# Kernel tuning notes

Hardware: AMD Instinct MI355X
Metric: run time of the kernel (lower is better)

The kernel has to match this reference:

```python
import jax, jax.numpy as jnp
import numpy as np

C_A = 768; C_S = 384; C_Z = 128; H = 16; D = C_A // H
B = 1; N = 4096; NQ = 32; NK = 128; NB = N // NQ
EPS = 1e-5


def _ln(x):
    # layernorm without learned affine (affine applied by caller where present)
    m = jnp.mean(x, axis=-1, keepdims=True)
    v = jnp.mean((x - m) ** 2, axis=-1, keepdims=True)
    return (x - m) * jax.lax.rsqrt(v + EPS)


def setup_inputs() -> dict:
    key = jax.random.key(0)
    ks = jax.random.split(key, 16)
    w = lambda k, shp: jax.random.normal(k, shp, dtype=jnp.float32) * 0.02
    return dict(
        a=jax.random.normal(ks[0], (B, N, C_A), jnp.float32),
        s=jax.random.normal(ks[1], (B, N, C_S), jnp.float32),
        z=jax.random.normal(ks[2], (B, NB, NQ, NK, C_Z), jnp.float32),
        adaln_gamma_s=jnp.ones((C_S,), jnp.float32),
        adaln_ws=w(ks[3], (C_S, C_A)),
        adaln_bs=jnp.zeros((C_A,), jnp.float32),
        adaln_wskip=w(ks[4], (C_S, C_A)),
        lnz_gamma=jnp.ones((C_Z,), jnp.float32),
        wz=w(ks[5], (C_Z, H)),
        wq=w(ks[6], (C_A, C_A)), bq=jnp.zeros((C_A,), jnp.float32),
        wk=w(ks[7], (C_A, C_A)),
        wv=w(ks[8], (C_A, C_A)),
        wg=w(ks[9], (C_A, C_A)), bg=jnp.ones((C_A,), jnp.float32),
        wo=w(ks[10], (C_A, C_A)), bo=jnp.zeros((C_A,), jnp.float32),
        w_last=w(ks[11], (C_S, C_A)),
        b_last=jnp.full((C_A,), -2.0, jnp.float32),  # biasinit = -2.0
        n_queries=NQ, n_keys=NK,
    )


def _forward(a, s, z, adaln_gamma_s, adaln_ws, adaln_bs, adaln_wskip,
             lnz_gamma, wz, wq, bq, wk, wv, wg, bg, wo, bo,
             w_last, b_last, n_queries, n_keys):
    Bq, Nq, _ = a.shape
    nb = Nq // n_queries
    # AdaptiveLayerNorm (AF3 Alg 26): a <- sigmoid(Lin(s_ln)) * LN(a) + LinNoBias(s_ln)
    s_ln = _ln(s) * adaln_gamma_s
    a_ln = jax.nn.sigmoid(s_ln @ adaln_ws + adaln_bs) * _ln(a) + s_ln @ adaln_wskip
    # pair bias: LN(z) (no offset) -> per-head bias, permuted to [B,H,nb,nq,nk]
    bias = (_ln(z) * lnz_gamma) @ wz                    # [B, nb, nq, nk, H]
    bias = jnp.transpose(bias, (0, 4, 1, 2, 3))          # [B, H, nb, nq, nk]
    # projections (q has bias; k/v no bias)
    q = (a_ln @ wq + bq).reshape(Bq, nb, n_queries, H, D)
    k = (a_ln @ wk).reshape(Bq, Nq, H, D)
    v = (a_ln @ wv).reshape(Bq, Nq, H, D)
    # local window: query block w covers [w*nq, (w+1)*nq); keys are nk centered on it
    start = jnp.arange(nb) * n_queries + n_queries // 2 - n_keys // 2
    kidx = start[:, None] + jnp.arange(n_keys)[None, :]  # [nb, nk]
    valid = (kidx >= 0) & (kidx < Nq)
    kidx = jnp.clip(kidx, 0, Nq - 1)
    k_loc = k[:, kidx]                                    # [B, nb, nk, H, D]
    v_loc = v[:, kidx]
    scale = 1.0 / float(np.sqrt(D))
    scores = jnp.einsum('bwqhd,bwkhd->bhwqk', q, k_loc) * scale + bias
    scores = jnp.where(valid[None, None, :, None, :], scores, -1e9)
    p = jax.nn.softmax(scores, axis=-1)
    o = jnp.einsum('bhwqk,bwkhd->bwqhd', p, v_loc).reshape(Bq, Nq, C_A)
    # gating, output projection, final sigmoid gate from raw s
    o = (jax.nn.sigmoid(a_ln @ wg + bg) * o) @ wo + bo
    return jax.nn.sigmoid(s @ w_last + b_last) * o


def reference(a, s, z, adaln_gamma_s, adaln_ws, adaln_bs, adaln_wskip,
              lnz_gamma, wz, wq, bq, wk, wv, wg, bg, wo, bo,
              w_last, b_last, n_queries, n_keys):
    return _forward(a, s, z, adaln_gamma_s, adaln_ws, adaln_bs, adaln_wskip,
                    lnz_gamma, wz, wq, bq, wk, wv, wg, bg, wo, bo,
                    w_last, b_last, n_queries, n_keys)
```

## Files before the change

### kernel.cpp

```cpp
#include <hip/hip_runtime.h>
#include <hip/hip_bf16.h>
#include <math.h>

#define N_TOK 4096
#define CA 768
#define CS 384
#define CZ 128
#define NHEAD 16
#define DH 48
#define NQW 32
#define NKW 128
#define NBLK 128

typedef __attribute__((ext_vector_type(8))) short short8;
typedef __attribute__((ext_vector_type(4))) float float4v;
typedef __attribute__((ext_vector_type(4))) unsigned short ushort4v;

__device__ __forceinline__ float sigmoidf_(float x){ return 1.0f/(1.0f+__expf(-x)); }

__device__ __forceinline__ unsigned short f2bf(float x){
  unsigned u = __float_as_uint(x);
  unsigned r = (u + 0x7FFFu + ((u>>16)&1u)) >> 16;
  return (unsigned short)r;
}
__device__ __forceinline__ float bf2f(unsigned short b){
  return __uint_as_float(((unsigned)b)<<16);
}
__device__ __forceinline__ short8 cvt8(const float* xv){
  union { short8 v; unsigned short u[8]; } H;
  #pragma unroll
  for (int j=0;j<8;j++) H.u[j] = f2bf(xv[j]);
  return H.v;
}
__device__ __forceinline__ short8 cvt8pk(const float* x){
  union { short8 v; unsigned u32[4]; } H;
  #pragma unroll
  for (int i=0;i<4;i++)
    asm("v_cvt_pk_bf16_f32 %0, %1, %2" : "=v"(H.u32[i]) : "v"(x[2*i]), "v"(x[2*i+1]));
  return H.v;
}

__device__ __forceinline__ void gload_lds16(const void* gsrc, void* ldst){
  __builtin_amdgcn_global_load_lds(
    (const __attribute__((address_space(1))) void*)gsrc,
    (__attribute__((address_space(3))) void*)ldst, 16, 0, 0);
}

__device__ __forceinline__ int xcd_swz(int wg, int nwg){
  int cpx = nwg >> 3;
  return (wg & 7)*cpx + (wg >> 3);
}

__global__ __launch_bounds__(256) void prep_zbias_kernel(
  const float* __restrict__ z, const float* __restrict__ lnz_gamma,
  const float* __restrict__ wz, unsigned short* __restrict__ bias3,
  const float* __restrict__ s, const float* __restrict__ adaln_gamma,
  unsigned short* __restrict__ s_ln_h, unsigned short* __restrict__ s_h,
  const float* __restrict__ a, float* __restrict__ a_n,
  const float* __restrict__ ws, const float* __restrict__ wskip,
  const float* __restrict__ wq, const float* __restrict__ wk,
  const float* __restrict__ wv, const float* __restrict__ wg,
  const float* __restrict__ wo, const float* __restrict__ wlast,
  unsigned short* __restrict__ Wt1, unsigned short* __restrict__ Wt2,
  unsigned short* __restrict__ Wt3, unsigned short* __restrict__ Wt4,
  const float* __restrict__ bq, const float* __restrict__ bg,
  float* __restrict__ biasq)
{
  union PZ {
    float tile[64][65];
    float zbuf[2][2][2048];
  };
  __shared__ PZ sm;
  int bid = blockIdx.x;
  int tid = threadIdx.x;

  if (bid < 2048){
    int wave = tid>>6, lane = tid&63;
    if (wave >= 2) return;
    int lr = lane&15, quad = lane>>4;

    short8 bwh[4];
    float w1 = 0.f;
    #pragma unroll
    for (int ks=0;ks<4;ks++){
      float wv_[8];
      #pragma unroll
      for (int j=0;j<8;j++){
        int k = ks*32 + quad*8 + j;
        wv_[j] = wz[k*NHEAD + lr]*lnz_gamma[k];
        w1 += wv_[j];
      }
      bwh[ks] = cvt8pk(wv_);
    }
    w1 += __shfl_xor(w1, 16);
    w1 += __shfl_xor(w1, 32);

    size_t group = (size_t)bid*2 + wave;
    const float* zg = z + group*(size_t)(NKW*CZ);
    unsigned short* outg = bias3 + group*2048;

    int rsub = lane>>5;
    int csw  = lane&31;
    auto stage = [&](int buf, int b){
      #pragma unroll
      for (int i=0;i<8;i++){
        int r  = 2*i + rsub;
        int gc = csw ^ (r & 7);
        gload_lds16(zg + (size_t)(b*16 + r)*CZ + gc*4, &sm.zbuf[wave][buf][i*256]);
      }
    };

    stage(0, 0);
    int buf = 0;
    #pragma unroll 1
    for (int b=0; b<8; ++b){
      if (b < 7){
        stage(buf^1, b+1);
        asm volatile("s_waitcnt vmcnt(8)" ::: "memory");
      } else {
        asm volatile("s_waitcnt vmcnt(0)" ::: "memory");
      }
      __builtin_amdgcn_sched_barrier(0);

      const float* rowp = &sm.zbuf[wave][buf][lr*128];
      int sswz = lr & 7;
      float4 p[8];
      #pragma unroll
      for (int ks=0;ks<4;ks++){
        int c0 = ks*8 + quad*2;
        p[ks*2]   = *(const float4*)(rowp + (size_t)((c0  )^sswz)*4);
        p[ks*2+1] = *(const float4*)(rowp + (size_t)((c0+1)^sswz)*4);
      }
      float sum=0.f, sq=0.f;
      #pragma unroll
      for (int t=0;t<8;t++){
        sum += p[t].x + p[t].y + p[t].z + p[t].w;
        sq  += p[t].x*p[t].x + p[t].y*p[t].y + p[t].z*p[t].z + p[t].w*p[t].w;
      }
      sum += __shfl_xor(sum,16); sum += __shfl_xor(sum,32);
      sq  += __shfl_xor(sq,16);  sq  += __shfl_xor(sq,32);
      float mean = sum*(1.f/CZ);
      float var  = sq*(1.f/CZ) - mean*mean;
      float rs = rsqrtf(var + 1e-5f);

      float4v c = (float4v){0.f,0.f,0.f,0.f};
      #pragma unroll
      for (int ks=0;ks<4;ks++){
        float xv[8];
        xv[0]=p[ks*2].x;   xv[1]=p[ks*2].y;   xv[2]=p[ks*2].z;   xv[3]=p[ks*2].w;
        xv[4]=p[ks*2+1].x; xv[5]=p[ks*2+1].y; xv[6]=p[ks*2+1].z; xv[7]=p[ks*2+1].w;
        c = __builtin_amdgcn_mfma_f32_16x16x32_bf16(cvt8pk(xv), bwh[ks], c, 0,0,0);
      }

      ushort4v o4;
      #pragma unroll
      for (int r=0;r<4;r++){
        int rrow = quad*4 + r;
        float m_r  = __shfl(mean, rrow);
        float rs_r = __shfl(rs, rrow);
        o4[r] = f2bf(rs_r*(c[r] - m_r*w1));
      }
      *(ushort4v*)(outg + lr*128 + b*16 + quad*4) = o4;
      buf ^= 1;
    }
    return;
  }
  bid -= 2048;

  if (bid < 1024){
    int wave = tid>>6, lane = tid&63;
    int row = bid*4 + wave;
    const float* x = s + (size_t)row*CS;
    float v[6]; float sum=0.f, sq=0.f;
    #pragma unroll
    for (int i=0;i<6;i++){ v[i]=x[lane+64*i]; sum+=v[i]; sq+=v[i]*v[i]; }
    #pragma unroll
    for (int off=32; off; off>>=1){ sum+=__shfl_xor(sum,off); sq+=__shfl_xor(sq,off); }
    float m = sum*(1.f/CS);
    float var = sq*(1.f/CS)-m*m;
    float rs = rsqrtf(var+1e-5f);
    #pragma unroll
    for (int i=0;i<6;i++){
      int c = lane+64*i;
      s_ln_h[(size_t)row*CS+c] = f2bf((v[i]-m)*rs*adaln_gamma[c]);
      s_h[(size_t)row*CS+c]    = f2bf(v[i]);
    }
    return;
  }
  bid -= 1024;

  if (bid < 1024){
    int wave = tid>>6, lane = tid&63;
    int row = bid*4 + wave;
    const float* x = a + (size_t)row*CA;
    float v[12]; float sum=0.f, sq=0.f;
    #pragma unroll
    for (int i=0;i<12;i++){ v[i]=x[lane+64*i]; sum+=v[i]; sq+=v[i]*v[i]; }
    #pragma unroll
    for (int off=32; off; off>>=1){ sum+=__shfl_xor(sum,off); sq+=__shfl_xor(sq,off); }
    float m = sum*(1.f/CA);
    float var = sq*(1.f/CA)-m*m;
    float rs = rsqrtf(var+1e-5f);
    float* o = a_n + (size_t)row*CA;
    #pragma unroll
    for (int i=0;i<12;i++) o[lane+64*i] = (v[i]-m)*rs;
    return;
  }
  bid -= 1024;

  if (bid < 936){
    const float* src; unsigned short* dst; int K; int local;
    if      (bid < 72)  { src=ws;    dst=Wt1;                   K=CS; local=bid; }
    else if (bid < 144) { src=wskip; dst=Wt1 + (size_t)768*CS;  K=CS; local=bid-72; }
    else if (bid < 288) { src=wq;    dst=Wt2;                   K=CA; local=bid-144; }
    else if (bid < 432) { src=wk;    dst=Wt2 + (size_t)768*CA;  K=CA; local=bid-288; }
    else if (bid < 576) { src=wv;    dst=Wt2 + (size_t)1536*CA; K=CA; local=bid-432; }
    else if (bid < 720) { src=wg;    dst=Wt2 + (size_t)2304*CA; K=CA; local=bid-576; }
    else if (bid < 864) { src=wo;    dst=Wt3;                   K=CA; local=bid-720; }
    else                { src=wlast; dst=Wt4;                   K=CS; local=bid-864; }
    int ktiles = K/64;
    int kb = (local % ktiles)*64, nb = (local / ktiles)*64;
    int c = tid & 63, r0 = tid >> 6;
    #pragma unroll
    for (int i=0;i<16;i++){
      int r = r0 + 4*i;
      sm.tile[r][c] = src[(size_t)(kb+r)*CA + nb + c];
    }
    __syncthreads();
    #pragma unroll
    for (int i=0;i<16;i++){
      int r = r0 + 4*i;
      dst[(size_t)(nb+r)*K + kb + c] = f2bf(sm.tile[c][r]);
    }
    return;
  }
  bid -= 936;

  int i = bid*256 + tid;
  float v = 0.f;
  if (i < 768) v = bq[i];
  else if (i >= 2304) v = bg[i-2304];
  biasq[i] = v;
}

__global__ __launch_bounds__(256) void adaln_gemm(
  const unsigned short* __restrict__ A, const unsigned short* __restrict__ Bt,
  const float* __restrict__ bs, const float* __restrict__ a_n,
  unsigned short* __restrict__ outh)
{
  __shared__ unsigned short Ash[64*64];
  __shared__ unsigned short B1sh[128*64];
  __shared__ unsigned short B2sh[128*64];

  int tid = threadIdx.x;
  int w = tid >> 6, lane = tid & 63;
  int lr = lane & 15, quad = lane >> 4;
  int wg = xcd_swz(blockIdx.y*gridDim.x + blockIdx.x, gridDim.x*gridDim.y);
  int bx = wg % gridDim.x, by = wg / gridDim.x;
  int m0 = by*64, n0 = bx*128;
  int mbase = (w&1)*32, nbase = (w>>1)*64;

  float4v acc1[2][4], acc2[2][4];
  #pragma unroll
  for (int i=0;i<2;i++)
    #pragma unroll
    for (int j=0;j<4;j++){
      acc1[i][j] = (float4v){0.f,0.f,0.f,0.f};
      acc2[i][j] = (float4v){0.f,0.f,0.f,0.f};
    }

  int rsub = lane>>3;
  int gcs  = ((lane&7) ^ rsub)*8;
  int rkey = lr & 7;

  for (int k0=0; k0<CS; k0+=64){
    __syncthreads();
    #pragma unroll
    for (int it=0; it<2; ++it){
      int r = it*32 + w*8 + rsub;
      gload_lds16(A + (size_t)(m0 + r)*CS + k0 + gcs, &Ash[(it*32 + w*8)*64]);
    }
    #pragma unroll
    for (int it=0; it<4; ++it){
      int r = it*32 + w*8 + rsub;
      gload_lds16(Bt + (size_t)(n0 + r)*CS + k0 + gcs, &B1sh[(it*32 + w*8)*64]);
      gload_lds16(Bt + (size_t)(768 + n0 + r)*CS + k0 + gcs, &B2sh[(it*32 + w*8)*64]);
    }
    __syncthreads();

    #pragma unroll
    for (int ks=0; ks<2; ++ks){
      int slot = ((ks*4 + quad) ^ rkey)*8;
      short8 af[2], b1f[4], b2f[4];
      #pragma unroll
      for (int mi=0;mi<2;mi++)
        af[mi] = *(const short8*)&Ash[(mbase + mi*16 + lr)*64 + slot];
      #pragma unroll
      for (int ni=0;ni<4;ni++){
        b1f[ni] = *(const short8*)&B1sh[(nbase + ni*16 + lr)*64 + slot];
        b2f[ni] = *(const short8*)&B2sh[(nbase + ni*16 + lr)*64 + slot];
      }
      #pragma unroll
      for (int mi=0;mi<2;mi++)
        #pragma unroll
        for (int ni=0;ni<4;ni++){
          acc1[mi][ni] = __builtin_amdgcn_mfma_f32_16x16x32_bf16(af[mi], b1f[ni], acc1[mi][ni], 0,0,0);
          acc2[mi][ni] = __builtin_amdgcn_mfma_f32_16x16x32_bf16(af[mi], b2f[ni], acc2[mi][ni], 0,0,0);
        }
    }
  }

  #pragma unroll
  for (int ni=0;ni<4;ni++){
    int col = n0 + nbase + ni*16 + lr;
    float bsv = bs[col];
    #pragma unroll
    for (int mi=0;mi<2;mi++){
      #pragma unroll
      for (int reg=0;reg<4;reg++){
        int row = m0 + mbase + mi*16 + quad*4 + reg;
        float v = sigmoidf_(acc1[mi][ni][reg] + bsv)*a_n[(size_t)row*CA + col] + acc2[mi][ni][reg];
        outh[(size_t)row*CA + col] = f2bf(v);
      }
    }
  }
}

__global__ __launch_bounds__(256) void final_gemm(
  const unsigned short* __restrict__ A1, const unsigned short* __restrict__ B1,
  const float* __restrict__ bias1,
  const unsigned short* __restrict__ A2, const unsigned short* __restrict__ B2,
  const float* __restrict__ bias2,
  float* __restrict__ outp)
{
  __shared__ unsigned short Ash[64*64];
  __shared__ unsigned short Bsh[128*64];

  int tid = threadIdx.x;
  int w = tid >> 6, lane = tid & 63;
  int lr = lane & 15, quad = lane >> 4;
  int wg = xcd_swz(blockIdx.y*gridDim.x + blockIdx.x, gridDim.x*gridDim.y);
  int bx = wg % gridDim.x, by = wg / gridDim.x;
  int m0 = by*64, n0 = bx*128;
  int mbase = (w&1)*32, nbase = (w>>1)*64;

  float4v acc1[2][4], acc2[2][4];
  #pragma unroll
  for (int i=0;i<2;i++)
    #pragma unroll
    for (int j=0;j<4;j++){
      acc1[i][j] = (float4v){0.f,0.f,0.f,0.f};
      acc2[i][j] = (float4v){0.f,0.f,0.f,0.f};
    }

  int rsub = lane>>3;
  int gcs  = ((lane&7) ^ rsub)*8;
  int rkey = lr & 7;

  const int NT1 = CA/64, NT2 = CS/64, NT = NT1+NT2;
  #pragma unroll 1
  for (int t=0; t<NT; ++t){
    const unsigned short* Ap; const unsigned short* Bp; int K, k0;
    if (t < NT1){ Ap=A1; Bp=B1; K=CA; k0=t*64; }
    else        { Ap=A2; Bp=B2; K=CS; k0=(t-NT1)*64; }
    __syncthreads();
    #pragma unroll
    for (int it=0; it<2; ++it){
      int r = it*32 + w*8 + rsub;
      gload_lds16(Ap + (size_t)(m0 + r)*K + k0 + gcs, &Ash[(it*32 + w*8)*64]);
    }
    #pragma unroll
    for (int it=0; it<4; ++it){
      int r = it*32 + w*8 + rsub;
      gload_lds16(Bp + (size_t)(n0 + r)*K + k0 + gcs, &Bsh[(it*32 + w*8)*64]);
    }
    __syncthreads();

    #pragma unroll
    for (int ks=0; ks<2; ++ks){
      int slot = ((ks*4 + quad) ^ rkey)*8;
      short8 af[2], bf[4];
      #pragma unroll
      for (int mi=0;mi<2;mi++)
        af[mi] = *(const short8*)&Ash[(mbase + mi*16 + lr)*64 + slot];
      #pragma unroll
      for (int ni=0;ni<4;ni++)
        bf[ni] = *(const short8*)&Bsh[(nbase + ni*16 + lr)*64 + slot];
      if (t < NT1){
        #pragma unroll
        for (int mi=0;mi<2;mi++)
          #pragma unroll
          for (int ni=0;ni<4;ni++)
            acc1[mi][ni] = __builtin_amdgcn_mfma_f32_16x16x32_bf16(af[mi], bf[ni], acc1[mi][ni], 0,0,0);
      } else {
        #pragma unroll
        for (int mi=0;mi<2;mi++)
          #pragma unroll
          for (int ni=0;ni<4;ni++)
            acc2[mi][ni] = __builtin_amdgcn_mfma_f32_16x16x32_bf16(af[mi], bf[ni], acc2[mi][ni], 0,0,0);
      }
    }
  }

  #pragma unroll
  for (int ni=0;ni<4;ni++){
    int col = n0 + nbase + ni*16 + lr;
    float bv1 = bias1[col];
    float bv2 = bias2[col];
    #pragma unroll
    for (int mi=0;mi<2;mi++){
      #pragma unroll
      for (int reg=0;reg<4;reg++){
        int row = m0 + mbase + mi*16 + quad*4 + reg;
        outp[(size_t)row*CA + col] = sigmoidf_(acc2[mi][ni][reg] + bv2)*(acc1[mi][ni][reg] + bv1);
      }
    }
  }
}

__global__ __launch_bounds__(512) void qkvg_gemm256(
  const unsigned short* __restrict__ A1, const unsigned short* __restrict__ B1,
  const float* __restrict__ bias1, unsigned short* __restrict__ outp)
{
  __shared__ unsigned short Ash[2][256*64];
  __shared__ unsigned short Bsh[2][256*64];

  int tid = threadIdx.x;
  int v = tid >> 6, lane = tid & 63;
  int lr = lane & 15, quad = lane >> 4;
  int wg = xcd_swz(blockIdx.y*gridDim.x + blockIdx.x, gridDim.x*gridDim.y);
  int bx = wg % gridDim.x, by = wg / gridDim.x;
  int m0 = by*256, n0 = bx*256;
  int wr = (v>>2)*128;
  int wc = (v&3)*64;

  float4v acc[8][4];
  #pragma unroll
  for (int i=0;i<8;i++)
    #pragma unroll
    for (int j=0;j<4;j++)
      acc[i][j] = (float4v){0.f,0.f,0.f,0.f};

  int rsub = lane>>3;
  int gcs  = ((lane&7) ^ rsub)*8;
  int rkey = lr & 7;

  const int NT = CA/64;

  auto stage = [&](int buf, int t){
    int k0 = t*64;
    #pragma unroll
    for (int i=0;i<4;i++){
      int R = i*64 + v*8;
      gload_lds16(A1 + (size_t)(m0 + R + rsub)*CA + k0 + gcs, &Ash[buf][R*64]);
      gload_lds16(B1 + (size_t)(n0 + R + rsub)*CA + k0 + gcs, &Bsh[buf][R*64]);
    }
  };

  stage(0, 0);
  stage(1, 1);
  int cur = 0;
  #pragma unroll 1
  for (int t=0; t<NT; ++t){
    if (t+1 < NT) asm volatile("s_waitcnt vmcnt(8)" ::: "memory");
    else          asm volatile("s_waitcnt vmcnt(0)" ::: "memory");
    __builtin_amdgcn_sched_barrier(0);
    __builtin_amdgcn_s_barrier();
    #pragma unroll
    for (int ks=0; ks<2; ++ks){
      int slot = ((ks*4 + quad) ^ rkey)*8;
      short8 af[8], bf[4];
      #pragma unroll
      for (int mi=0;mi<8;mi++)
        af[mi] = *(const short8*)&Ash[cur][(wr + mi*16 + lr)*64 + slot];
      #pragma unroll
      for (int ni=0;ni<4;ni++)
        bf[ni] = *(const short8*)&Bsh[cur][(wc + ni*16 + lr)*64 + slot];
      #pragma unroll
      for (int mi=0;mi<8;mi++)
        #pragma unroll
        for (int ni=0;ni<4;ni++)
          acc[mi][ni] = __builtin_amdgcn_mfma_f32_16x16x32_bf16(af[mi], bf[ni], acc[mi][ni], 0,0,0);
    }
    __builtin_amdgcn_s_barrier();
    if (t+2 < NT) stage(cur, t+2);
    cur ^= 1;
  }

  #pragma unroll
  for (int ni=0;ni<4;ni++){
    int col = n0 + wc + ni*16 + lr;
    float bv = bias1[col];
    #pragma unroll
    for (int mi=0;mi<8;mi++){
      #pragma unroll
      for (int reg=0;reg<4;reg++){
        int row = m0 + wr + mi*16 + quad*4 + reg;
        outp[(size_t)row*3072 + col] = f2bf(acc[mi][ni][reg] + bv);
      }
    }
  }
}

__global__ __launch_bounds__(256) void attn_kernel(
  const unsigned short* __restrict__ qh,
  const unsigned short* __restrict__ bias3h,
  unsigned short* __restrict__ og)
{
  __shared__ unsigned short Vs[128*192];
  __shared__ unsigned short Pb[4][32*40];
  int tid = threadIdx.x, wave = tid>>6, lane = tid&63;
  int lr = lane&15, quad = lane>>4;
  int w = blockIdx.x, h = blockIdx.y*4 + wave;
  int start = w*NQW - 48;
  const float scale = 0.14433756729740643f;

  {
    int hbase = blockIdx.y*4*DH;
    #pragma unroll
    for (int it=0; it<12; ++it){
      int c = it*256 + tid;
      int key = c/24, cc = c - key*24;
      int kr = min(max(start+key,0),N_TOK-1);
      short8 v = *(const short8*)&qh[(size_t)kr*3072 + 1536 + hbase + cc*8];
      int cs = cc ^ (((key>>3)&3)*2);
      *(short8*)&Vs[key*192 + cs*8] = v;
    }
  }

  short8 zero8 = {0,0,0,0,0,0,0,0};

  short8 aq[2][2];
  #pragma unroll
  for (int mt=0;mt<2;mt++){
    int row = w*NQW + mt*16 + lr;
    const unsigned short* qp = qh + (size_t)row*3072 + h*DH;
    aq[mt][0] = *(const short8*)(qp + quad*8);
    aq[mt][1] = (quad<2) ? *(const short8*)(qp + 32 + quad*8) : zero8;
  }

  float4v c[2][8];
  #pragma unroll
  for (int mt=0;mt<2;mt++)
    #pragma unroll
    for (int nt=0;nt<8;nt++) c[mt][nt] = (float4v){0.f,0.f,0.f,0.f};

  #pragma unroll 2
  for (int nt=0;nt<8;nt++){
    int krc = min(max(start + nt*16 + lr,0),N_TOK-1);
    const unsigned short* kp = qh + (size_t)krc*3072 + 768 + h*DH;
    short8 bk0 = *(const short8*)(kp + quad*8);
    short8 bk1 = (quad<2) ? *(const short8*)(kp + 32 + quad*8) : zero8;
    #pragma unroll
    for (int mt=0;mt<2;mt++){
      c[mt][nt] = __builtin_amdgcn_mfma_f32_16x16x32_bf16(aq[mt][0], bk0, c[mt][nt], 0,0,0);
      c[mt][nt] = __builtin_amdgcn_mfma_f32_16x16x32_bf16(aq[mt][1], bk1, c[mt][nt], 0,0,0);
    }
  }

  float rmax[2][4], rsum[2][4];
  #pragma unroll
  for (int mt=0;mt<2;mt++)
    #pragma unroll
    for (int r=0;r<4;r++){ rmax[mt][r] = -3.0e38f; rsum[mt][r] = 0.f; }

  #pragma unroll
  for (int nt=0;nt<8;nt++){
    int key = start + nt*16 + lr;
    bool valid = (key>=0) && (key<N_TOK);
    #pragma unroll
    for (int mt=0;mt<2;mt++){
      #pragma unroll
      for (int r=0;r<4;r++){
        int q = mt*16 + quad*4 + r;
        float bv = bf2f(bias3h[(((size_t)(w*NQW+q))*NHEAD + h)*128 + nt*16 + lr]);
        float v = valid ? (c[mt][nt][r]*scale + bv) : -1e9f;
        c[mt][nt][r] = v;
        rmax[mt][r] = fmaxf(rmax[mt][r], v);
      }
    }
  }
  #pragma unroll
  for (int mt=0;mt<2;mt++)
    #pragma unroll
    for (int r=0;r<4;r++){
      float m = rmax[mt][r];
      m = fmaxf(m, __shfl_xor(m,1)); m = fmaxf(m, __shfl_xor(m,2));
      m = fmaxf(m, __shfl_xor(m,4)); m = fmaxf(m, __shfl_xor(m,8));
      rmax[mt][r] = m;
    }
  #pragma unroll
  for (int nt=0;nt<8;nt++)
    #pragma unroll
    for (int mt=0;mt<2;mt++)
      #pragma unroll
      for (int r=0;r<4;r++){
        float e = __expf(c[mt][nt][r] - rmax[mt][r]);
        c[mt][nt][r] = e;
        rsum[mt][r] += e;
      }
  #pragma unroll
  for (int mt=0;mt<2;mt++)
    #pragma unroll
    for (int r=0;r<4;r++){
      float sv = rsum[mt][r];
      sv += __shfl_xor(sv,1); sv += __shfl_xor(sv,2);
      sv += __shfl_xor(sv,4); sv += __shfl_xor(sv,8);
      rsum[mt][r] = 1.f/sv;
    }

  __syncthreads();

  unsigned short* ph = &Pb[wave][0];
  float4v o[2][3];
  #pragma unroll
  for (int mt=0;mt<2;mt++)
    #pragma unroll
    for (int no=0;no<3;no++) o[mt][no] = (float4v){0.f,0.f,0.f,0.f};

  #pragma unroll 1
  for (int c2=0;c2<2;c2++){
    #pragma unroll 1
    for (int ks=0;ks<2;ks++){
      int ntb = c2*4 + ks*2;
      #pragma unroll
      for (int t=0;t<2;t++){
        int nt = ntb + t;
        #pragma unroll
        for (int mt=0;mt<2;mt++){
          #pragma unroll
          for (int r=0;r<4;r++){
            int q = mt*16 + quad*4 + r;
            ph[q*40 + t*16 + lr] = f2bf(c[mt][nt][r]*rsum[mt][r]);
          }
        }
      }
      short8 pa[2];
      #pragma unroll
      for (int mt=0;mt<2;mt++)
        pa[mt] = *(const short8*)&ph[(mt*16+lr)*40 + quad*8];
      #pragma unroll
      for (int no=0;no<3;no++){
        union { short8 v; unsigned short u[8]; } V;
        int col = wave*DH + no*16 + lr;
        int chunk = col >> 3;
        int cs = (chunk ^ (quad*2))*8 + (col & 7);
        #pragma unroll
        for (int j=0;j<8;j++){
          int key = c2*64 + ks*32 + quad*8 + j;
          V.u[j] = Vs[key*192 + cs];
        }
        #pragma unroll
        for (int mt=0;mt<2;mt++)
          o[mt][no] = __builtin_amdgcn_mfma_f32_16x16x32_bf16(pa[mt], V.v, o[mt][no], 0,0,0);
      }
    }
  }

  #pragma unroll
  for (int mt=0;mt<2;mt++){
    #pragma unroll
    for (int no=0;no<3;no++){
      int d = no*16 + lr;
      #pragma unroll
      for (int r=0;r<4;r++){
        int q = mt*16 + quad*4 + r;
        size_t grow = (size_t)(w*NQW + q);
        float g = bf2f(qh[grow*3072 + 2304 + h*DH + d]);
        og[grow*CA + h*DH + d] = f2bf(o[mt][no][r] * sigmoidf_(g));
      }
    }
  }
}

extern "C" void kernel_launch(void* const* d_in, const int* in_sizes, int n_in,
                              void* d_out, int out_size, void* d_ws, size_t ws_size,
                              hipStream_t stream)
{
  const float* a            = (const float*)d_in[0];
  const float* s            = (const float*)d_in[1];
  const float* z            = (const float*)d_in[2];
  const float* adaln_gamma  = (const float*)d_in[3];
  const float* adaln_ws     = (const float*)d_in[4];
  const float* adaln_bs     = (const float*)d_in[5];
  const float* adaln_wskip  = (const float*)d_in[6];
  const float* lnz_gamma    = (const float*)d_in[7];
  const float* wz           = (const float*)d_in[8];
  const float* wq           = (const float*)d_in[9];
  const float* bq           = (const float*)d_in[10];
  const float* wk           = (const float*)d_in[11];
  const float* wv           = (const float*)d_in[12];
  const float* wg           = (const float*)d_in[13];
  const float* bg           = (const float*)d_in[14];
  const float* wo           = (const float*)d_in[15];
  const float* bo           = (const float*)d_in[16];
  const float* w_last       = (const float*)d_in[17];
  const float* b_last       = (const float*)d_in[18];
  float* out = (float*)d_out;

  char* base = (char*)d_ws;
  size_t off = 0;
  auto alloc = [&](size_t bytes)->char*{ char* p = base + off; off += (bytes + 255) & ~(size_t)255; return p; };

  unsigned short* s_ln_h = (unsigned short*)alloc((size_t)N_TOK*CS*2);
  unsigned short* s_h    = (unsigned short*)alloc((size_t)N_TOK*CS*2);
  float*          a_n    = (float*)alloc((size_t)N_TOK*CA*4);
  unsigned short* a_ln_h = (unsigned short*)alloc((size_t)N_TOK*CA*2);
  unsigned short* og_h   = (unsigned short*)alloc((size_t)N_TOK*CA*2);
  unsigned short* Wt1    = (unsigned short*)alloc((size_t)1536*CS*2);
  unsigned short* Wt2    = (unsigned short*)alloc((size_t)3072*CA*2);
  unsigned short* Wt3    = (unsigned short*)alloc((size_t)CA*CA*2);
  unsigned short* Wt4    = (unsigned short*)alloc((size_t)CA*CS*2);
  unsigned short* bias3h = (unsigned short*)alloc((size_t)N_TOK*NHEAD*NKW*2);
  unsigned short* qkvg_h = (unsigned short*)alloc((size_t)N_TOK*3072*2);
  float*          biasq  = (float*)alloc((size_t)3072*4);

  prep_zbias_kernel<<<dim3(2048+1024+1024+936+12), 256, 0, stream>>>(
      z, lnz_gamma, wz, bias3h,
      s, adaln_gamma, s_ln_h, s_h, a, a_n,
      adaln_ws, adaln_wskip, wq, wk, wv, wg, wo, w_last,
      Wt1, Wt2, Wt3, Wt4, bq, bg, biasq);

  adaln_gemm<<<dim3(CA/128, N_TOK/64), 256, 0, stream>>>(s_ln_h, Wt1, adaln_bs, a_n, a_ln_h);

  qkvg_gemm256<<<dim3(3072/256, N_TOK/256), 512, 0, stream>>>(a_ln_h, Wt2, biasq, qkvg_h);

  attn_kernel<<<dim3(NBLK, 4), 256, 0, stream>>>(qkvg_h, bias3h, og_h);

  final_gemm<<<dim3(CA/128, N_TOK/64), 256, 0, stream>>>(
      og_h, Wt3, bo, s_h, Wt4, b_last, out);
}
```

Before: 217.6 us.

## Move z-bias LayerNorm projection into the AdaLN GEMM launch

The pair-bias computation (LayerNorm of z times wz) moves out of the prep kernel into the same launch as the AdaLN GEMM, with the z blocks placed after the 384 GEMM tiles. This shortens the prep kernel on the critical path and lets the bandwidth-bound z streaming overlap the compute-bound AdaLN GEMM. The shared-memory union now has to cover the GEMM buffers as well, which raises LDS per block and may lower occupancy for the z blocks.

```diff
diff --git a/kernel.cpp b/kernel.cpp
--- a/kernel.cpp
+++ b/kernel.cpp
@@ -51,9 +51,7 @@
   return (wg & 7)*cpx + (wg >> 3);
 }
 
-__global__ __launch_bounds__(256) void prep_zbias_kernel(
-  const float* __restrict__ z, const float* __restrict__ lnz_gamma,
-  const float* __restrict__ wz, unsigned short* __restrict__ bias3,
+__global__ __launch_bounds__(256) void prep_fast_kernel(
   const float* __restrict__ s, const float* __restrict__ adaln_gamma,
   unsigned short* __restrict__ s_ln_h, unsigned short* __restrict__ s_h,
   const float* __restrict__ a, float* __restrict__ a_n,
@@ -66,106 +64,9 @@
   const float* __restrict__ bq, const float* __restrict__ bg,
   float* __restrict__ biasq)
 {
-  union PZ {
-    float tile[64][65];
-    float zbuf[2][2][2048];
-  };
-  __shared__ PZ sm;
+  __shared__ float tile[64][65];
   int bid = blockIdx.x;
   int tid = threadIdx.x;
-
-  if (bid < 2048){
-    int wave = tid>>6, lane = tid&63;
-    if (wave >= 2) return;
-    int lr = lane&15, quad = lane>>4;
-
-    short8 bwh[4];
-    float w1 = 0.f;
-    #pragma unroll
-    for (int ks=0;ks<4;ks++){
-      float wv_[8];
-      #pragma unroll
-      for (int j=0;j<8;j++){
-        int k = ks*32 + quad*8 + j;
-        wv_[j] = wz[k*NHEAD + lr]*lnz_gamma[k];
-        w1 += wv_[j];
-      }
-      bwh[ks] = cvt8pk(wv_);
-    }
-    w1 += __shfl_xor(w1, 16);
-    w1 += __shfl_xor(w1, 32);
-
-    size_t group = (size_t)bid*2 + wave;
-    const float* zg = z + group*(size_t)(NKW*CZ);
-    unsigned short* outg = bias3 + group*2048;
-
-    int rsub = lane>>5;
-    int csw  = lane&31;
-    auto stage = [&](int buf, int b){
-      #pragma unroll
-      for (int i=0;i<8;i++){
-        int r  = 2*i + rsub;
-        int gc = csw ^ (r & 7);
-        gload_lds16(zg + (size_t)(b*16 + r)*CZ + gc*4, &sm.zbuf[wave][buf][i*256]);
-      }
-    };
-
-    stage(0, 0);
-    int buf = 0;
-    #pragma unroll 1
-    for (int b=0; b<8; ++b){
-      if (b < 7){
-        stage(buf^1, b+1);
-        asm volatile("s_waitcnt vmcnt(8)" ::: "memory");
-      } else {
-        asm volatile("s_waitcnt vmcnt(0)" ::: "memory");
-      }
-      __builtin_amdgcn_sched_barrier(0);
-
-      const float* rowp = &sm.zbuf[wave][buf][lr*128];
-      int sswz = lr & 7;
-      float4 p[8];
-      #pragma unroll
-      for (int ks=0;ks<4;ks++){
-        int c0 = ks*8 + quad*2;
-        p[ks*2]   = *(const float4*)(rowp + (size_t)((c0  )^sswz)*4);
-        p[ks*2+1] = *(const float4*)(rowp + (size_t)((c0+1)^sswz)*4);
-      }
-      float sum=0.f, sq=0.f;
-      #pragma unroll
-      for (int t=0;t<8;t++){
-        sum += p[t].x + p[t].y + p[t].z + p[t].w;
-        sq  += p[t].x*p[t].x + p[t].y*p[t].y + p[t].z*p[t].z + p[t].w*p[t].w;
-      }
-      sum += __shfl_xor(sum,16); sum += __shfl_xor(sum,32);
-      sq  += __shfl_xor(sq,16);  sq  += __shfl_xor(sq,32);
-      float mean = sum*(1.f/CZ);
-      float var  = sq*(1.f/CZ) - mean*mean;
-      float rs = rsqrtf(var + 1e-5f);
-
-      float4v c = (float4v){0.f,0.f,0.f,0.f};
-      #pragma unroll
-      for (int ks=0;ks<4;ks++){
-        float xv[8];
-        xv[0]=p[ks*2].x;   xv[1]=p[ks*2].y;   xv[2]=p[ks*2].z;   xv[3]=p[ks*2].w;
-        xv[4]=p[ks*2+1].x; xv[5]=p[ks*2+1].y; xv[6]=p[ks*2+1].z; xv[7]=p[ks*2+1].w;
-        c = __builtin_amdgcn_mfma_f32_16x16x32_bf16(cvt8pk(xv), bwh[ks], c, 0,0,0);
-      }
-
-      ushort4v o4;
-      #pragma unroll
-      for (int r=0;r<4;r++){
-        int rrow = quad*4 + r;
-        float m_r  = __shfl(mean, rrow);
-        float rs_r = __shfl(rs, rrow);
-        o4[r] = f2bf(rs_r*(c[r] - m_r*w1));
-      }
-      *(ushort4v*)(outg + lr*128 + b*16 + quad*4) = o4;
-      buf ^= 1;
-    }
-    return;
-  }
-  bid -= 2048;
 
   if (bid < 1024){
     int wave = tid>>6, lane = tid&63;
@@ -224,13 +125,13 @@
     #pragma unroll
     for (int i=0;i<16;i++){
       int r = r0 + 4*i;
-      sm.tile[r][c] = src[(size_t)(kb+r)*CA + nb + c];
+      tile[r][c] = src[(size_t)(kb+r)*CA + nb + c];
     }
     __syncthreads();
     #pragma unroll
     for (int i=0;i<16;i++){
       int r = r0 + 4*i;
-      dst[(size_t)(nb+r)*K + kb + c] = f2bf(sm.tile[c][r]);
+      dst[(size_t)(nb+r)*K + kb + c] = f2bf(tile[c][r]);
     }
     return;
   }
@@ -243,86 +144,183 @@
   biasq[i] = v;
 }
 
-__global__ __launch_bounds__(256) void adaln_gemm(
+__global__ __launch_bounds__(256) void zbias_adaln_kernel(
+  const float* __restrict__ z, const float* __restrict__ lnz_gamma,
+  const float* __restrict__ wz, unsigned short* __restrict__ bias3,
   const unsigned short* __restrict__ A, const unsigned short* __restrict__ Bt,
   const float* __restrict__ bs, const float* __restrict__ a_n,
   unsigned short* __restrict__ outh)
 {
-  __shared__ unsigned short Ash[64*64];
-  __shared__ unsigned short B1sh[128*64];
-  __shared__ unsigned short B2sh[128*64];
-
+  union ZA {
+    struct { unsigned short Ash[64*64], B1sh[128*64], B2sh[128*64]; } g;
+    float zbuf[2][2][2048];
+  };
+  __shared__ ZA sm;
+  int bid = blockIdx.x;
   int tid = threadIdx.x;
-  int w = tid >> 6, lane = tid & 63;
-  int lr = lane & 15, quad = lane >> 4;
-  int wg = xcd_swz(blockIdx.y*gridDim.x + blockIdx.x, gridDim.x*gridDim.y);
-  int bx = wg % gridDim.x, by = wg / gridDim.x;
-  int m0 = by*64, n0 = bx*128;
-  int mbase = (w&1)*32, nbase = (w>>1)*64;
-
-  float4v acc1[2][4], acc2[2][4];
-  #pragma unroll
-  for (int i=0;i<2;i++)
-    #pragma unroll
-    for (int j=0;j<4;j++){
-      acc1[i][j] = (float4v){0.f,0.f,0.f,0.f};
-      acc2[i][j] = (float4v){0.f,0.f,0.f,0.f};
-    }
-
-  int rsub = lane>>3;
-  int gcs  = ((lane&7) ^ rsub)*8;
-  int rkey = lr & 7;
-
-  for (int k0=0; k0<CS; k0+=64){
-    __syncthreads();
-    #pragma unroll
-    for (int it=0; it<2; ++it){
-      int r = it*32 + w*8 + rsub;
-      gload_lds16(A + (size_t)(m0 + r)*CS + k0 + gcs, &Ash[(it*32 + w*8)*64]);
-    }
-    #pragma unroll
-    for (int it=0; it<4; ++it){
-      int r = it*32 + w*8 + rsub;
-      gload_lds16(Bt + (size_t)(n0 + r)*CS + k0 + gcs, &B1sh[(it*32 + w*8)*64]);
-      gload_lds16(Bt + (size_t)(768 + n0 + r)*CS + k0 + gcs, &B2sh[(it*32 + w*8)*64]);
-    }
-    __syncthreads();
-
-    #pragma unroll
-    for (int ks=0; ks<2; ++ks){
-      int slot = ((ks*4 + quad) ^ rkey)*8;
-      short8 af[2], b1f[4], b2f[4];
-      #pragma unroll
-      for (int mi=0;mi<2;mi++)
-        af[mi] = *(const short8*)&Ash[(mbase + mi*16 + lr)*64 + slot];
-      #pragma unroll
-      for (int ni=0;ni<4;ni++){
-        b1f[ni] = *(const short8*)&B1sh[(nbase + ni*16 + lr)*64 + slot];
-        b2f[ni] = *(const short8*)&B2sh[(nbase + ni*16 + lr)*64 + slot];
-      }
-      #pragma unroll
-      for (int mi=0;mi<2;mi++)
+  int wave = tid>>6, lane = tid&63;
+  int lr = lane&15, quad = lane>>4;
+
+  if (bid < 384){
+    int w = wave;
+    int wg = xcd_swz(bid, 384);
+    int bx = wg % 6, by = wg / 6;
+    int m0 = by*64, n0 = bx*128;
+    int mbase = (w&1)*32, nbase = (w>>1)*64;
+
+    float4v acc1[2][4], acc2[2][4];
+    #pragma unroll
+    for (int i=0;i<2;i++)
+      #pragma unroll
+      for (int j=0;j<4;j++){
+        acc1[i][j] = (float4v){0.f,0.f,0.f,0.f};
+        acc2[i][j] = (float4v){0.f,0.f,0.f,0.f};
+      }
+
+    int rsub = lane>>3;
+    int gcs  = ((lane&7) ^ rsub)*8;
+    int rkey = lr & 7;
+
+    for (int k0=0; k0<CS; k0+=64){
+      __syncthreads();
+      #pragma unroll
+      for (int it=0; it<2; ++it){
+        int r = it*32 + w*8 + rsub;
+        gload_lds16(A + (size_t)(m0 + r)*CS + k0 + gcs, &sm.g.Ash[(it*32 + w*8)*64]);
+      }
+      #pragma unroll
+      for (int it=0; it<4; ++it){
+        int r = it*32 + w*8 + rsub;
+        gload_lds16(Bt + (size_t)(n0 + r)*CS + k0 + gcs, &sm.g.B1sh[(it*32 + w*8)*64]);
+        gload_lds16(Bt + (size_t)(768 + n0 + r)*CS + k0 + gcs, &sm.g.B2sh[(it*32 + w*8)*64]);
+      }
+      __syncthreads();
+
+      #pragma unroll
+      for (int ks=0; ks<2; ++ks){
+        int slot = ((ks*4 + quad) ^ rkey)*8;
+        short8 af[2], b1f[4], b2f[4];
+        #pragma unroll
+        for (int mi=0;mi<2;mi++)
+          af[mi] = *(const short8*)&sm.g.Ash[(mbase + mi*16 + lr)*64 + slot];
         #pragma unroll
         for (int ni=0;ni<4;ni++){
-          acc1[mi][ni] = __builtin_amdgcn_mfma_f32_16x16x32_bf16(af[mi], b1f[ni], acc1[mi][ni], 0,0,0);
-          acc2[mi][ni] = __builtin_amdgcn_mfma_f32_16x16x32_bf16(af[mi], b2f[ni], acc2[mi][ni], 0,0,0);
+          b1f[ni] = *(const short8*)&sm.g.B1sh[(nbase + ni*16 + lr)*64 + slot];
+          b2f[ni] = *(const short8*)&sm.g.B2sh[(nbase + ni*16 + lr)*64 + slot];
         }
-    }
-  }
-
-  #pragma unroll
-  for (int ni=0;ni<4;ni++){
-    int col = n0 + nbase + ni*16 + lr;
-    float bsv = bs[col];
-    #pragma unroll
-    for (int mi=0;mi<2;mi++){
-      #pragma unroll
-      for (int reg=0;reg<4;reg++){
-        int row = m0 + mbase + mi*16 + quad*4 + reg;
-        float v = sigmoidf_(acc1[mi][ni][reg] + bsv)*a_n[(size_t)row*CA + col] + acc2[mi][ni][reg];
-        outh[(size_t)row*CA + col] = f2bf(v);
-      }
-    }
+        #pragma unroll
+        for (int mi=0;mi<2;mi++)
+          #pragma unroll
+          for (int ni=0;ni<4;ni++){
+            acc1[mi][ni] = __builtin_amdgcn_mfma_f32_16x16x32_bf16(af[mi], b1f[ni], acc1[mi][ni], 0,0,0);
+            acc2[mi][ni] = __builtin_amdgcn_mfma_f32_16x16x32_bf16(af[mi], b2f[ni], acc2[mi][ni], 0,0,0);
+          }
+      }
+    }
+
+    #pragma unroll
+    for (int ni=0;ni<4;ni++){
+      int col = n0 + nbase + ni*16 + lr;
+      float bsv = bs[col];
+      #pragma unroll
+      for (int mi=0;mi<2;mi++){
+        #pragma unroll
+        for (int reg=0;reg<4;reg++){
+          int row = m0 + mbase + mi*16 + quad*4 + reg;
+          float v = sigmoidf_(acc1[mi][ni][reg] + bsv)*a_n[(size_t)row*CA + col] + acc2[mi][ni][reg];
+          outh[(size_t)row*CA + col] = f2bf(v);
+        }
+      }
+    }
+    return;
+  }
+  bid -= 384;
+
+  if (wave >= 2) return;
+
+  short8 bwh[4];
+  float w1 = 0.f;
+  #pragma unroll
+  for (int ks=0;ks<4;ks++){
+    float wv_[8];
+    #pragma unroll
+    for (int j=0;j<8;j++){
+      int k = ks*32 + quad*8 + j;
+      wv_[j] = wz[k*NHEAD + lr]*lnz_gamma[k];
+      w1 += wv_[j];
+    }
+    bwh[ks] = cvt8pk(wv_);
+  }
+  w1 += __shfl_xor(w1, 16);
+  w1 += __shfl_xor(w1, 32);
+
+  size_t group = (size_t)bid*2 + wave;
+  const float* zg = z + group*(size_t)(NKW*CZ);
+  unsigned short* outg = bias3 + group*2048;
+
+  int rsub = lane>>5;
+  int csw  = lane&31;
+  auto stage = [&](int buf, int b){
+    #pragma unroll
+    for (int i=0;i<8;i++){
+      int r  = 2*i + rsub;
+      int gc = csw ^ (r & 7);
+      gload_lds16(zg + (size_t)(b*16 + r)*CZ + gc*4, &sm.zbuf[wave][buf][i*256]);
+    }
+  };
+
+  stage(0, 0);
+  int buf = 0;
+  #pragma unroll 1
+  for (int b=0; b<8; ++b){
+    if (b < 7){
+      stage(buf^1, b+1);
+      asm volatile("s_waitcnt vmcnt(8)" ::: "memory");
+    } else {
+      asm volatile("s_waitcnt vmcnt(0)" ::: "memory");
+    }
+    __builtin_amdgcn_sched_barrier(0);
+
+    const float* rowp = &sm.zbuf[wave][buf][lr*128];
+    int sswz = lr & 7;
+    float4 p[8];
+    #pragma unroll
+    for (int ks=0;ks<4;ks++){
+      int c0 = ks*8 + quad*2;
+      p[ks*2]   = *(const float4*)(rowp + (size_t)((c0  )^sswz)*4);
+      p[ks*2+1] = *(const float4*)(rowp + (size_t)((c0+1)^sswz)*4);
+    }
+    float sum=0.f, sq=0.f;
+    #pragma unroll
+    for (int t=0;t<8;t++){
+      sum += p[t].x + p[t].y + p[t].z + p[t].w;
+      sq  += p[t].x*p[t].x + p[t].y*p[t].y + p[t].z*p[t].z + p[t].w*p[t].w;
+    }
+    sum += __shfl_xor(sum,16); sum += __shfl_xor(sum,32);
+    sq  += __shfl_xor(sq,16);  sq  += __shfl_xor(sq,32);
+    float mean = sum*(1.f/CZ);
+    float var  = sq*(1.f/CZ) - mean*mean;
+    float rs = rsqrtf(var + 1e-5f);
+
+    float4v c = (float4v){0.f,0.f,0.f,0.f};
+    #pragma unroll
+    for (int ks=0;ks<4;ks++){
+      float xv[8];
+      xv[0]=p[ks*2].x;   xv[1]=p[ks*2].y;   xv[2]=p[ks*2].z;   xv[3]=p[ks*2].w;
+      xv[4]=p[ks*2+1].x; xv[5]=p[ks*2+1].y; xv[6]=p[ks*2+1].z; xv[7]=p[ks*2+1].w;
+      c = __builtin_amdgcn_mfma_f32_16x16x32_bf16(cvt8pk(xv), bwh[ks], c, 0,0,0);
+    }
+
+    ushort4v o4;
+    #pragma unroll
+    for (int r=0;r<4;r++){
+      int rrow = quad*4 + r;
+      float m_r  = __shfl(mean, rrow);
+      float rs_r = __shfl(rs, rrow);
+      o4[r] = f2bf(rs_r*(c[r] - m_r*w1));
+    }
+    *(ushort4v*)(outg + lr*128 + b*16 + quad*4) = o4;
+    buf ^= 1;
   }
 }
 
@@ -715,13 +713,14 @@
   unsigned short* qkvg_h = (unsigned short*)alloc((size_t)N_TOK*3072*2);
   float*          biasq  = (float*)alloc((size_t)3072*4);
 
-  prep_zbias_kernel<<<dim3(2048+1024+1024+936+12), 256, 0, stream>>>(
-      z, lnz_gamma, wz, bias3h,
+  prep_fast_kernel<<<dim3(1024+1024+936+12), 256, 0, stream>>>(
       s, adaln_gamma, s_ln_h, s_h, a, a_n,
       adaln_ws, adaln_wskip, wq, wk, wv, wg, wo, w_last,
       Wt1, Wt2, Wt3, Wt4, bq, bg, biasq);
 
-  adaln_gemm<<<dim3(CA/128, N_TOK/64), 256, 0, stream>>>(s_ln_h, Wt1, adaln_bs, a_n, a_ln_h);
+  zbias_adaln_kernel<<<dim3(384+2048), 256, 0, stream>>>(
+      z, lnz_gamma, wz, bias3h,
+      s_ln_h, Wt1, adaln_bs, a_n, a_ln_h);
 
   qkvg_gemm256<<<dim3(3072/256, N_TOK/256), 512, 0, stream>>>(a_ln_h, Wt2, biasq, qkvg_h);
 
```

Measured after the change: 225.9 us. 1.04x slower.
